# Kernel optimization log

Measured on AMD Instinct MI355X. Metric: run time of the kernel, lower is better.

## Reference

```python
import jax, jax.numpy as jnp
import numpy as np

N, D, E = 100000, 128, 1600000
BN_SCALE = 1.0 / np.sqrt(1.0 + 1e-3)  # Keras BN at inference with init stats: x/sqrt(var+eps)


def bn(x):
    return x * jnp.asarray(BN_SCALE, x.dtype)


def l2norm(x):
    s = jnp.sum(x * x, axis=1, keepdims=True)
    return x * jax.lax.rsqrt(jnp.maximum(s, 1e-12))


def spmm(rows, cols, vals, h, n):
    # (sparse NxN) @ (dense NxD) via gather + segment_sum
    return jax.ops.segment_sum(vals[:, None] * h[cols], rows, num_segments=n)


def setup_inputs() -> dict:
    key = jax.random.key(0)
    ks = jax.random.split(key, 12)
    g = 1.0 / np.sqrt(D)  # glorot-ish scale
    return {
        "x": jax.random.normal(ks[0], (N, D), jnp.float32),
        "a1_rows": jax.random.randint(ks[1], (E,), 0, N, jnp.int32),
        "a1_cols": jax.random.randint(ks[2], (E,), 0, N, jnp.int32),
        "a1_vals": jax.random.uniform(ks[3], (E,), jnp.float32),
        "a2_rows": jax.random.randint(ks[4], (E,), 0, N, jnp.int32),
        "a2_cols": jax.random.randint(ks[5], (E,), 0, N, jnp.int32),
        "a2_vals": jnp.ones((E,), jnp.float32),
        "w_gcn1": jax.random.normal(ks[6], (D, D), jnp.float32) * g,
        "b_gcn1": jnp.zeros((D,), jnp.float32),
        "w_att": jax.random.normal(ks[7], (D, D), jnp.float32) * g,
        "m1": jax.random.normal(ks[8], (D, D), jnp.float32) * g,
        "m2": jax.random.normal(ks[9], (D, D), jnp.float32) * g,
        "w_hw": jax.random.normal(ks[10], (D, D), jnp.float32) * g,
        "w_gcn2": jax.random.normal(ks[11], (D, D), jnp.float32) * g,
        "b_gcn2": jnp.zeros((D,), jnp.float32),
    }


def gcn_layer(x, rows, cols, vals, w, b, n):
    xb = bn(x)
    return jnp.tanh(spmm(rows, cols, vals, xb @ w, n) + b)


def atten_layer(x, rows, cols, vals, w, m1, m2, n):
    xb = bn(x)
    mapped = xb @ w  # [N, D]
    s1 = jnp.tanh(jnp.sum((xb @ m1) * xb, axis=1))  # [N]
    s2 = jnp.tanh(jnp.sum((xb @ m2) * xb, axis=1))  # [N]
    # per-edge score: A*s1[row] + A^T-broadcast s2[col], then leaky_relu (tf alpha=0.2)
    e = jax.nn.leaky_relu(vals * s1[rows] + vals * s2[cols], negative_slope=0.2)
    # sparse row-wise softmax
    mx = jax.ops.segment_max(e, rows, num_segments=n)
    ex = jnp.exp(e - mx[rows])
    denom = jax.ops.segment_sum(ex, rows, num_segments=n)
    a = ex / denom[rows]
    return spmm(rows, cols, a / jnp.maximum(vals, 1e-30) * vals * 0 + a, mapped, n) if False else jax.ops.segment_sum(a[:, None] * mapped[cols], rows, num_segments=n)


def highway_layer(y_att, y_gcn, w):
    i1 = bn(y_att)
    i2 = bn(y_gcn)
    gate = jax.nn.relu(jnp.tanh(i1 @ w))
    return jnp.tanh(i2 * (1.0 - gate) + i1 * gate)


def reference(x, a1_rows, a1_cols, a1_vals, a2_rows, a2_cols, a2_vals,
              w_gcn1, b_gcn1, w_att, m1, m2, w_hw, w_gcn2, b_gcn2):
    n = x.shape[0]
    y1 = gcn_layer(x, a1_rows, a1_cols, a1_vals, w_gcn1, b_gcn1, n)
    y2 = atten_layer(x, a2_rows, a2_cols, a2_vals, w_att, m1, m2, n)
    y3 = highway_layer(y2, y1, w_hw)
    y4 = gcn_layer(y3, a1_rows, a1_cols, a1_vals, w_gcn2, b_gcn2, n)
    y = jnp.concatenate([l2norm(y3), l2norm(y4), l2norm(x)], axis=1)
    return l2norm(y)
```

## Files before the change

kernel.cpp:

```cpp
#include <hip/hip_runtime.h>
#include <hip/hip_fp16.h>
#include <math.h>
#include <stdint.h>

#define DD 128
#define BSH 9

typedef _Float16 f16;
typedef _Float16 f16x8 __attribute__((ext_vector_type(8)));
typedef float f32x4 __attribute__((ext_vector_type(4)));

__global__ void k_hist(const int* __restrict__ r1, const int* __restrict__ r2,
                       int* __restrict__ hist, int E, int tile, int nt){
  __shared__ int h1[256], h2[256];
  int t = threadIdx.x;
  h1[t]=0; h2[t]=0; __syncthreads();
  int e0 = blockIdx.x*tile, e1 = min(e0+tile, E);
  for(int e=e0+t; e<e1; e+=256){
    atomicAdd(&h1[r1[e]>>BSH], 1);
    atomicAdd(&h2[r2[e]>>BSH], 1);
  }
  __syncthreads();
  hist[(size_t)blockIdx.x*256 + t] = h1[t];
  hist[(size_t)nt*256 + (size_t)blockIdx.x*256 + t] = h2[t];
}

__global__ void k_colscan(int* __restrict__ hist, int* __restrict__ colsum, int nt){
  __shared__ int sh[256];
  int g = blockIdx.x>>8, b = blockIdx.x&255;
  int t = threadIdx.x;
  int* H = hist + (size_t)g*nt*256;
  int v = (t<nt)? H[(size_t)t*256+b] : 0;
  sh[t]=v; __syncthreads();
  for(int off=1; off<256; off<<=1){
    int add = (t>=off)? sh[t-off] : 0;
    __syncthreads(); sh[t]+=add; __syncthreads();
  }
  if(t<nt) H[(size_t)t*256+b] = sh[t]-v;
  if(t==255) colsum[g*256+b] = sh[255];
}

__global__ void k_basescan(const int* __restrict__ colsum, int* __restrict__ base){
  __shared__ int sh[512];
  int t = threadIdx.x;
  int g = t>>8, st = t&255;
  int v = colsum[t];
  sh[t]=v; __syncthreads();
  for(int off=1; off<256; off<<=1){
    int add = (st>=off)? sh[t-off] : 0;
    __syncthreads(); sh[t]+=add; __syncthreads();
  }
  base[g*257+st] = sh[t]-v;
  if(st==255) base[g*257+256] = sh[t];
}

__global__ void k_partition(const int* __restrict__ r1, const int* __restrict__ c1, const float* __restrict__ v1,
                            const int* __restrict__ r2, const int* __restrict__ c2,
                            const int* __restrict__ hist, const int* __restrict__ base,
                            int2* __restrict__ st1, int* __restrict__ st2, int E, int tile, int nt){
  __shared__ int l1[256], l2[256];
  int t = threadIdx.x;
  l1[t]=0; l2[t]=0; __syncthreads();
  int bx = blockIdx.x;
  int e0 = bx*tile, e1e = min(e0+tile, E);
  const int* off1 = hist + (size_t)bx*256;
  const int* off2 = hist + (size_t)nt*256 + (size_t)bx*256;
  for(int e=e0+t; e<e1e; e+=256){
    {
      int r = r1[e]; int b = r>>BSH;
      int rank = atomicAdd(&l1[b], 1);
      int dst = base[b] + off1[b] + rank;
      st1[dst] = make_int2(((r - (b<<BSH))<<17) | c1[e], __float_as_int(v1[e]));
    }
    {
      int r = r2[e]; int b = r>>BSH;
      int rank = atomicAdd(&l2[b], 1);
      int dst = base[257+b] + off2[b] + rank;
      st2[dst] = ((r - (b<<BSH))<<17) | c2[e];
    }
  }
}

__global__ void k_csr_bucket(const int2* __restrict__ st1, const int* __restrict__ st2,
                             const int* __restrict__ base,
                             int2* __restrict__ e1, int* __restrict__ e2,
                             int* __restrict__ rs, int N, int nbk){
  __shared__ int cnt[512];
  __shared__ int cur[512];
  __shared__ int sc[256];
  int g = blockIdx.x / nbk;
  int b = blockIdx.x % nbk;
  int t = threadIdx.x;
  cnt[t]=0; cnt[256+t]=0;
  __syncthreads();
  int ebeg = base[g*257+b], eend = base[g*257+b+1];
  if(g==0){
    for(int i=ebeg+t; i<eend; i+=256) atomicAdd(&cnt[st1[i].x>>17], 1);
  } else {
    for(int i=ebeg+t; i<eend; i+=256) atomicAdd(&cnt[st2[i]>>17], 1);
  }
  __syncthreads();
  int a0 = cnt[2*t], a1 = cnt[2*t+1];
  int s = a0+a1;
  sc[t]=s; __syncthreads();
  for(int off=1; off<256; off<<=1){
    int add = (t>=off)? sc[t-off] : 0;
    __syncthreads(); sc[t]+=add; __syncthreads();
  }
  int ex = sc[t]-s;
  cur[2*t] = ex; cur[2*t+1] = ex + a0;
  __syncthreads();
  int r0 = b<<BSH;
  int* rsg = rs + (size_t)g*(N+1);
  for(int i=t; i<512; i+=256){
    int r = r0+i;
    if(r<N) rsg[r] = ebeg + cur[i];
  }
  if(b==nbk-1 && t==0) rsg[N] = base[g*257+256];
  __syncthreads();
  if(g==0){
    for(int i=ebeg+t; i<eend; i+=256){
      int2 w = st1[i];
      int lr = w.x>>17;
      int p = ebeg + atomicAdd(&cur[lr], 1);
      e1[p] = make_int2(w.x & 0x1FFFF, w.y);
    }
  } else {
    for(int i=ebeg+t; i<eend; i+=256){
      int w = st2[i];
      int lr = w>>17;
      int p = ebeg + atomicAdd(&cur[lr], 1);
      e2[p] = w & 0x1FFFF;
    }
  }
}

__global__ void k_wprep(const float* __restrict__ w0, const float* __restrict__ w1,
                        const float* __restrict__ w2, const float* __restrict__ w3,
                        const float* __restrict__ w4, const float* __restrict__ w5,
                        f16* __restrict__ wh){
  __shared__ __align__(16) f16 tw[128][136];
  int b = blockIdx.x, t = threadIdx.x;
  const float* W = (b==0)?w0:(b==1)?w1:(b==2)?w2:(b==3)?w3:(b==4)?w4:w5;
  for(int j=0;j<16;++j){
    int f = j*256+t; int k = f>>5, c4 = f&31;
    float4 v = *(const float4*)(W + (size_t)k*DD + c4*4);
    tw[c4*4+0][k]=(f16)v.x; tw[c4*4+1][k]=(f16)v.y; tw[c4*4+2][k]=(f16)v.z; tw[c4*4+3][k]=(f16)v.w;
  }
  __syncthreads();
  f16* dst = wh + (size_t)b*16384;
  for(int j=0;j<8;++j){
    int f = j*256+t; int c = f>>4, seg = f&15;
    *(int4*)&dst[(size_t)c*DD + seg*8] = *(int4*)&tw[c][seg*8];
  }
}

__global__ __launch_bounds__(256) void k_xgemms(
    const float* __restrict__ x, const f16* __restrict__ wh,
    f16* __restrict__ h1h, f16* __restrict__ mapped,
    float* __restrict__ s1, float* __restrict__ s2,
    float bn, float sscale, int n){
  __shared__ __align__(16) f16 at[64][136];
  __shared__ __align__(16) f16 wt[128][136];
  int t = threadIdx.x;
  int r0 = blockIdx.x*64;
  int l = t&63, w = t>>6, li = l&15, g = l>>4;
  for(int p=0;p<4;++p){
    int row = p*16 + (t>>4), seg = t&15;
    union{ f16 h[8]; int4 v; } u;
    u.v = make_int4(0,0,0,0);
    if(r0+row < n){
      const float* src = x + (size_t)(r0+row)*DD + seg*8;
      float4 a = *(const float4*)src, b = *(const float4*)(src+4);
      u.h[0]=(f16)a.x; u.h[1]=(f16)a.y; u.h[2]=(f16)a.z; u.h[3]=(f16)a.w;
      u.h[4]=(f16)b.x; u.h[5]=(f16)b.y; u.h[6]=(f16)b.z; u.h[7]=(f16)b.w;
    }
    *(int4*)&at[row][seg*8] = u.v;
  }
  for(int p=0;p<4;++p){
    __syncthreads();
    const f16* Wp = wh + (size_t)p*16384;
    for(int j=0;j<8;++j){
      int f = j*256+t; int c = f>>4, seg = f&15;
      *(int4*)&wt[c][seg*8] = *(const int4*)(Wp + (size_t)c*DD + seg*8);
    }
    __syncthreads();
    f32x4 acc[8];
    #pragma unroll
    for(int ct=0;ct<8;++ct) acc[ct] = (f32x4){0.f,0.f,0.f,0.f};
    #pragma unroll
    for(int ks=0;ks<4;++ks){
      f16x8 a = *(const f16x8*)&at[w*16+li][ks*32+g*8];
      #pragma unroll
      for(int ct=0;ct<8;++ct){
        f16x8 b = *(const f16x8*)&wt[ct*16+li][ks*32+g*8];
        acc[ct] = __builtin_amdgcn_mfma_f32_16x16x32_f16(a, b, acc[ct], 0,0,0);
      }
    }
    if(p<2){
      f16* out = p ? mapped : h1h;
      __syncthreads();
      #pragma unroll
      for(int ct=0;ct<8;++ct)
        #pragma unroll
        for(int reg=0;reg<4;++reg)
          wt[w*16+g*4+reg][ct*16+li] = (f16)(acc[ct][reg]*bn);
      __syncthreads();
      for(int j=0;j<4;++j){
        int f = j*256+t; int row = f>>4, seg = f&15;
        if(r0+row < n) *(int4*)&out[(size_t)(r0+row)*DD + seg*8] = *(int4*)&wt[row][seg*8];
      }
    } else {
      float* sd = (p==2) ? s1 : s2;
      #pragma unroll
      for(int reg=0;reg<4;++reg){
        float pd = 0.f;
        #pragma unroll
        for(int ct=0;ct<8;++ct)
          pd += acc[ct][reg]*(float)at[w*16+g*4+reg][ct*16+li];
        pd += __shfl_xor(pd,1,64); pd += __shfl_xor(pd,2,64);
        pd += __shfl_xor(pd,4,64); pd += __shfl_xor(pd,8,64);
        if(li==0){
          int grow = r0 + w*16 + g*4 + reg;
          if(grow < n) sd[grow] = tanhf(sscale*pd);
        }
      }
    }
  }
}

__global__ __launch_bounds__(256) void k_hw2(
    const f16* __restrict__ y2h, const f16* __restrict__ y1h,
    const f16* __restrict__ wh, f16* __restrict__ y3h, f16* __restrict__ h3h,
    float bn, int n){
  __shared__ __align__(16) f16 at[64][136];
  __shared__ __align__(16) f16 wt[128][136];
  int t = threadIdx.x;
  int r0 = blockIdx.x*64;
  int l = t&63, w = t>>6, li = l&15, g = l>>4;
  for(int p=0;p<4;++p){
    int row = p*16 + (t>>4), seg = t&15;
    int4 v = make_int4(0,0,0,0);
    if(r0+row < n) v = *(const int4*)(y2h + (size_t)(r0+row)*DD + seg*8);
    *(int4*)&at[row][seg*8] = v;
  }
  __syncthreads();
  for(int j=0;j<8;++j){
    int f = j*256+t; int c = f>>4, seg = f&15;
    *(int4*)&wt[c][seg*8] = *(const int4*)(wh + (size_t)4*16384 + (size_t)c*DD + seg*8);
  }
  __syncthreads();
  f32x4 acc[8];
  #pragma unroll
  for(int ct=0;ct<8;++ct) acc[ct] = (f32x4){0.f,0.f,0.f,0.f};
  #pragma unroll
  for(int ks=0;ks<4;++ks){
    f16x8 a = *(const f16x8*)&at[w*16+li][ks*32+g*8];
    #pragma unroll
    for(int ct=0;ct<8;++ct){
      f16x8 b = *(const f16x8*)&wt[ct*16+li][ks*32+g*8];
      acc[ct] = __builtin_amdgcn_mfma_f32_16x16x32_f16(a, b, acc[ct], 0,0,0);
    }
  }
  float res[8][4];
  #pragma unroll
  for(int ct=0;ct<8;++ct)
    #pragma unroll
    for(int reg=0;reg<4;++reg){
      int lrow = w*16+g*4+reg, col = ct*16+li;
      int grow = r0+lrow;
      float gt = tanhf(bn*acc[ct][reg]); gt = fmaxf(gt, 0.f);
      float y1v = (grow<n)? (float)y1h[(size_t)grow*DD+col] : 0.f;
      float y2v = (float)at[lrow][col];
      res[ct][reg] = tanhf(bn*(y1v*(1.f-gt) + y2v*gt));
    }
  #pragma unroll
  for(int ct=0;ct<8;++ct)
    #pragma unroll
    for(int reg=0;reg<4;++reg)
      at[w*16+g*4+reg][ct*16+li] = (f16)res[ct][reg];
  __syncthreads();
  for(int j=0;j<4;++j){
    int f = j*256+t; int row = f>>4, seg = f&15;
    if(r0+row < n) *(int4*)&y3h[(size_t)(r0+row)*DD + seg*8] = *(int4*)&at[row][seg*8];
  }
  __syncthreads();
  for(int j=0;j<8;++j){
    int f = j*256+t; int c = f>>4, seg = f&15;
    *(int4*)&wt[c][seg*8] = *(const int4*)(wh + (size_t)5*16384 + (size_t)c*DD + seg*8);
  }
  __syncthreads();
  #pragma unroll
  for(int ct=0;ct<8;++ct) acc[ct] = (f32x4){0.f,0.f,0.f,0.f};
  #pragma unroll
  for(int ks=0;ks<4;++ks){
    f16x8 a = *(const f16x8*)&at[w*16+li][ks*32+g*8];
    #pragma unroll
    for(int ct=0;ct<8;++ct){
      f16x8 b = *(const f16x8*)&wt[ct*16+li][ks*32+g*8];
      acc[ct] = __builtin_amdgcn_mfma_f32_16x16x32_f16(a, b, acc[ct], 0,0,0);
    }
  }
  __syncthreads();
  #pragma unroll
  for(int ct=0;ct<8;++ct)
    #pragma unroll
    for(int reg=0;reg<4;++reg)
      wt[w*16+g*4+reg][ct*16+li] = (f16)(acc[ct][reg]*bn);
  __syncthreads();
  for(int j=0;j<4;++j){
    int f = j*256+t; int row = f>>4, seg = f&15;
    if(r0+row < n) *(int4*)&h3h[(size_t)(r0+row)*DD + seg*8] = *(int4*)&wt[row][seg*8];
  }
}

__device__ __forceinline__ void spmm_row(const int* __restrict__ rs, const int2* __restrict__ e1,
                                         const __half* __restrict__ h, const float* __restrict__ bias,
                                         __half* __restrict__ out, int row, int lane){
  int beg = rs[row], end = rs[row+1];
  float ax=0.f, ay=0.f;
  int k = beg;
  for(; k+8<=end; k+=8){
    int2 cv[8]; __half2 hh[8];
    #pragma unroll
    for(int j=0;j<8;++j) cv[j] = e1[k+j];
    #pragma unroll
    for(int j=0;j<8;++j) hh[j] = ((const __half2*)(h + (size_t)cv[j].x*DD))[lane];
    #pragma unroll
    for(int j=0;j<8;++j){
      float v = __int_as_float(cv[j].y);
      float2 f = __half22float2(hh[j]);
      ax += v*f.x; ay += v*f.y;
    }
  }
  for(; k<end; ++k){
    int2 cv = e1[k];
    float v = __int_as_float(cv.y);
    float2 f = __half22float2(((const __half2*)(h + (size_t)cv.x*DD))[lane]);
    ax += v*f.x; ay += v*f.y;
  }
  float2 b = ((const float2*)bias)[lane];
  ((__half2*)(out + (size_t)row*DD))[lane] = __floats2half2_rn(tanhf(ax+b.x), tanhf(ay+b.y));
}

__device__ __forceinline__ void attn_row(const int* __restrict__ rs, const int* __restrict__ e2,
                                         const float* __restrict__ s1, const float* __restrict__ s2,
                                         const __half* __restrict__ mapped, __half* __restrict__ out,
                                         int row, int lane){
  int beg = rs[row], end = rs[row+1];
  float s1r = s1[row];
  float ax=0.f, ay=0.f, den=0.f;
  int k = beg;
  for(; k+8<=end; k+=8){
    int cs[8]; float sv[8]; __half2 mh[8];
    #pragma unroll
    for(int j=0;j<8;++j) cs[j] = e2[k+j];
    #pragma unroll
    for(int j=0;j<8;++j) sv[j] = s2[cs[j]];
    #pragma unroll
    for(int j=0;j<8;++j) mh[j] = ((const __half2*)(mapped + (size_t)cs[j]*DD))[lane];
    #pragma unroll
    for(int j=0;j<8;++j){
      float e = s1r + sv[j]; e = (e>=0.f)? e : 0.2f*e;
      float ex = __expf(e);
      float2 f = __half22float2(mh[j]);
      den += ex; ax += ex*f.x; ay += ex*f.y;
    }
  }
  for(; k<end; ++k){
    int c = e2[k];
    float e = s1r + s2[c]; e = (e>=0.f)? e : 0.2f*e;
    float ex = __expf(e);
    float2 f = __half22float2(((const __half2*)(mapped + (size_t)c*DD))[lane]);
    den += ex; ax += ex*f.x; ay += ex*f.y;
  }
  float inv = (end > beg) ? 1.0f/den : 0.0f;
  ((__half2*)(out + (size_t)row*DD))[lane] = __floats2half2_rn(ax*inv, ay*inv);
}

__global__ void k_agg1(const int* __restrict__ rs, const int2* __restrict__ e1,
                       const __half* __restrict__ h1h, const float* __restrict__ b1, __half* __restrict__ y1h,
                       const int* __restrict__ e2, const float* __restrict__ s1, const float* __restrict__ s2,
                       const __half* __restrict__ mapped, __half* __restrict__ y2h,
                       int n, int gR){
  int lane = threadIdx.x & 63;
  if((int)blockIdx.x < gR){
    int row = blockIdx.x*4 + (threadIdx.x>>6);
    if(row>=n) return;
    spmm_row(rs, e1, h1h, b1, y1h, row, lane);
  } else {
    int row = (blockIdx.x-gR)*4 + (threadIdx.x>>6);
    if(row>=n) return;
    attn_row(rs+(n+1), e2, s1, s2, mapped, y2h, row, lane);
  }
}

__global__ void k_spmm2(const int* __restrict__ rs, const int2* __restrict__ e1,
                        const __half* __restrict__ h, const float* __restrict__ bias,
                        __half* __restrict__ out, int n){
  int row = blockIdx.x*4 + (threadIdx.x>>6);
  if(row>=n) return;
  spmm_row(rs, e1, h, bias, out, row, threadIdx.x & 63);
}

__global__ void k_final(const __half* __restrict__ y3, const __half* __restrict__ y4,
                        const float* __restrict__ x, float* __restrict__ out, int n){
  int row = blockIdx.x*4 + (threadIdx.x>>6);
  if(row>=n) return;
  int lane = threadIdx.x & 63;
  float2 a = __half22float2(((const __half2*)(y3 + (size_t)row*DD))[lane]);
  float2 b = __half22float2(((const __half2*)(y4 + (size_t)row*DD))[lane]);
  float2 c = ((const float2*)(x  + (size_t)row*DD))[lane];
  float sa = a.x*a.x + a.y*a.y;
  float sb = b.x*b.x + b.y*b.y;
  float sc = c.x*c.x + c.y*c.y;
  #pragma unroll
  for(int off=32; off; off>>=1){
    sa += __shfl_xor(sa, off, 64);
    sb += __shfl_xor(sb, off, 64);
    sc += __shfl_xor(sc, off, 64);
  }
  float ia = rsqrtf(fmaxf(sa, 1e-12f));
  float ib = rsqrtf(fmaxf(sb, 1e-12f));
  float ic = rsqrtf(fmaxf(sc, 1e-12f));
  float tot = sa*ia*ia + sb*ib*ib + sc*ic*ic;
  float f = rsqrtf(fmaxf(tot, 1e-12f));
  float fa = ia*f, fb = ib*f, fc = ic*f;
  float2* o = (float2*)(out + (size_t)row*(3*DD));
  o[lane]     = make_float2(a.x*fa, a.y*fa);
  o[64+lane]  = make_float2(b.x*fb, b.y*fb);
  o[128+lane] = make_float2(c.x*fc, c.y*fc);
}

extern "C" void kernel_launch(void* const* d_in, const int* in_sizes, int n_in,
                              void* d_out, int out_size, void* d_ws, size_t ws_size,
                              hipStream_t stream){
  const float* x   = (const float*)d_in[0];
  const int*   a1r = (const int*)d_in[1];
  const int*   a1c = (const int*)d_in[2];
  const float* a1v = (const float*)d_in[3];
  const int*   a2r = (const int*)d_in[4];
  const int*   a2c = (const int*)d_in[5];
  const float* w1  = (const float*)d_in[7];
  const float* b1  = (const float*)d_in[8];
  const float* watt= (const float*)d_in[9];
  const float* m1  = (const float*)d_in[10];
  const float* m2  = (const float*)d_in[11];
  const float* whw = (const float*)d_in[12];
  const float* w2  = (const float*)d_in[13];
  const float* b2  = (const float*)d_in[14];

  const int N = in_sizes[0]/DD;
  const int E = in_sizes[1];
  const float BN = (float)(1.0/sqrt(1.0+1e-3));
  const size_t NB = (size_t)N*DD;

  int tile = 8192, nt = (E+tile-1)/tile;
  while(nt > 256){ tile <<= 1; nt = (E+tile-1)/tile; }
  const int nbk = (N + (1<<BSH) - 1) >> BSH;

  f16* Bh = (f16*)d_ws;
  f16* Ch = Bh + NB;
  f16* Dh = Ch + NB;
  f16* Eh = Dh + NB;
  f16* wh = Eh + NB;
  float* s1 = (float*)(wh + 6*16384);
  float* s2 = s1 + N;
  int*  rs  = (int*)(s2 + N);
  uintptr_t pa = ((uintptr_t)(rs + 2*(N+1)) + 15) & ~(uintptr_t)15;
  int2* e1  = (int2*)pa;
  int*  e2  = (int*)(e1 + E);
  int*  hist = e2 + E;
  int*  colsum = hist + (size_t)2*nt*256;
  int*  base = colsum + 512;

  int2* st1 = (int2*)Bh;
  int*  st2 = (int*)(st1 + E);

  const int gR = (N+3)/4;
  const int gM = (N+63)/64;
  float* out = (float*)d_out;

  k_wprep<<<6,256,0,stream>>>(w1, watt, m1, m2, whw, w2, wh);

  k_hist<<<nt,256,0,stream>>>(a1r, a2r, hist, E, tile, nt);
  k_colscan<<<512,256,0,stream>>>(hist, colsum, nt);
  k_basescan<<<1,512,0,stream>>>(colsum, base);
  k_partition<<<nt,256,0,stream>>>(a1r,a1c,a1v, a2r,a2c, hist, base, st1, st2, E, tile, nt);
  k_csr_bucket<<<2*nbk,256,0,stream>>>(st1, st2, base, e1, e2, rs, N, nbk);

  k_xgemms<<<gM,256,0,stream>>>(x, wh, Bh, Ch, s1, s2, BN, BN*BN, N);

  k_agg1<<<2*gR,256,0,stream>>>(rs, e1, (const __half*)Bh, b1, (__half*)Dh,
                                e2, s1, s2, (const __half*)Ch, (__half*)Eh, N, gR);

  k_hw2<<<gM,256,0,stream>>>(Eh, Dh, wh, Ch, Bh, BN, N);

  k_spmm2<<<gR,256,0,stream>>>(rs, e1, (const __half*)Bh, b2, (__half*)Dh, N);

  k_final<<<gR,256,0,stream>>>((const __half*)Ch, (const __half*)Dh, x, out, N);
}
```

Before: 497.3 us.

## Co-schedule weight prep with histogram and GEMMs with partition; half-wave row aggregation

Merges the weight-conversion kernel into the histogram launch and the dense x-GEMM kernel into the edge-partition launch, using block-index ranges so independent work shares one grid. The partition staging buffers move out of the Bh region into their own workspace so the GEMM can write Bh at the same time. SpMM and attention aggregation now use 32 lanes per row with 8-byte loads and 8 rows per block, and handle the tail with clamped, masked loads instead of a scalar remainder loop. This cuts launch count and idle tail time and raises per-lane memory width. In exchange it uses more workspace memory and does some wasted loads on partial batches.

```diff
diff --git a/kernel.cpp b/kernel.cpp
--- a/kernel.cpp
+++ b/kernel.cpp
@@ -10,19 +10,42 @@
 typedef _Float16 f16x8 __attribute__((ext_vector_type(8)));
 typedef float f32x4 __attribute__((ext_vector_type(4)));
 
-__global__ void k_hist(const int* __restrict__ r1, const int* __restrict__ r2,
-                       int* __restrict__ hist, int E, int tile, int nt){
-  __shared__ int h1[256], h2[256];
+__global__ __launch_bounds__(256) void k_ph(
+    const float* __restrict__ w0, const float* __restrict__ w1, const float* __restrict__ w2,
+    const float* __restrict__ w3, const float* __restrict__ w4, const float* __restrict__ w5,
+    f16* __restrict__ wh,
+    const int* __restrict__ r1, const int* __restrict__ r2, int* __restrict__ hist,
+    int E, int tile, int nt){
+  __shared__ __align__(16) unsigned char smem[128*136*2];
   int t = threadIdx.x;
-  h1[t]=0; h2[t]=0; __syncthreads();
-  int e0 = blockIdx.x*tile, e1 = min(e0+tile, E);
-  for(int e=e0+t; e<e1; e+=256){
-    atomicAdd(&h1[r1[e]>>BSH], 1);
-    atomicAdd(&h2[r2[e]>>BSH], 1);
-  }
-  __syncthreads();
-  hist[(size_t)blockIdx.x*256 + t] = h1[t];
-  hist[(size_t)nt*256 + (size_t)blockIdx.x*256 + t] = h2[t];
+  if((int)blockIdx.x < 6){
+    auto tw = (f16 (*)[136])smem;
+    int b = blockIdx.x;
+    const float* W = (b==0)?w0:(b==1)?w1:(b==2)?w2:(b==3)?w3:(b==4)?w4:w5;
+    for(int j=0;j<16;++j){
+      int f = j*256+t; int k = f>>5, c4 = f&31;
+      float4 v = *(const float4*)(W + (size_t)k*DD + c4*4);
+      tw[c4*4+0][k]=(f16)v.x; tw[c4*4+1][k]=(f16)v.y; tw[c4*4+2][k]=(f16)v.z; tw[c4*4+3][k]=(f16)v.w;
+    }
+    __syncthreads();
+    f16* dst = wh + (size_t)b*16384;
+    for(int j=0;j<8;++j){
+      int f = j*256+t; int c = f>>4, seg = f&15;
+      *(int4*)&dst[(size_t)c*DD + seg*8] = *(int4*)&tw[c][seg*8];
+    }
+  } else {
+    int* h1 = (int*)smem; int* h2 = h1+256;
+    h1[t]=0; h2[t]=0; __syncthreads();
+    int hb = blockIdx.x - 6;
+    int e0 = hb*tile, e1 = min(e0+tile, E);
+    for(int e=e0+t; e<e1; e+=256){
+      atomicAdd(&h1[r1[e]>>BSH], 1);
+      atomicAdd(&h2[r2[e]>>BSH], 1);
+    }
+    __syncthreads();
+    hist[(size_t)hb*256 + t] = h1[t];
+    hist[(size_t)nt*256 + (size_t)hb*256 + t] = h2[t];
+  }
 }
 
 __global__ void k_colscan(int* __restrict__ hist, int* __restrict__ colsum, int nt){
@@ -54,29 +77,104 @@
   if(st==255) base[g*257+256] = sh[t];
 }
 
-__global__ void k_partition(const int* __restrict__ r1, const int* __restrict__ c1, const float* __restrict__ v1,
-                            const int* __restrict__ r2, const int* __restrict__ c2,
-                            const int* __restrict__ hist, const int* __restrict__ base,
-                            int2* __restrict__ st1, int* __restrict__ st2, int E, int tile, int nt){
-  __shared__ int l1[256], l2[256];
+__global__ __launch_bounds__(256) void k_px(
+    const int* __restrict__ r1, const int* __restrict__ c1, const float* __restrict__ v1,
+    const int* __restrict__ r2, const int* __restrict__ c2,
+    const int* __restrict__ hist, const int* __restrict__ base,
+    int2* __restrict__ st1, int* __restrict__ st2, int E, int tile, int nt,
+    const float* __restrict__ x, const f16* __restrict__ wh,
+    f16* __restrict__ h1h, f16* __restrict__ mapped,
+    float* __restrict__ s1, float* __restrict__ s2,
+    float bn, float sscale, int n){
+  __shared__ __align__(16) unsigned char smem[52224];
   int t = threadIdx.x;
-  l1[t]=0; l2[t]=0; __syncthreads();
-  int bx = blockIdx.x;
-  int e0 = bx*tile, e1e = min(e0+tile, E);
-  const int* off1 = hist + (size_t)bx*256;
-  const int* off2 = hist + (size_t)nt*256 + (size_t)bx*256;
-  for(int e=e0+t; e<e1e; e+=256){
-    {
-      int r = r1[e]; int b = r>>BSH;
-      int rank = atomicAdd(&l1[b], 1);
-      int dst = base[b] + off1[b] + rank;
-      st1[dst] = make_int2(((r - (b<<BSH))<<17) | c1[e], __float_as_int(v1[e]));
-    }
-    {
-      int r = r2[e]; int b = r>>BSH;
-      int rank = atomicAdd(&l2[b], 1);
-      int dst = base[257+b] + off2[b] + rank;
-      st2[dst] = ((r - (b<<BSH))<<17) | c2[e];
+  if((int)blockIdx.x < nt){
+    int* l1 = (int*)smem; int* l2 = l1+256;
+    l1[t]=0; l2[t]=0; __syncthreads();
+    int bx = blockIdx.x;
+    int e0 = bx*tile, e1e = min(e0+tile, E);
+    const int* off1 = hist + (size_t)bx*256;
+    const int* off2 = hist + (size_t)nt*256 + (size_t)bx*256;
+    for(int e=e0+t; e<e1e; e+=256){
+      {
+        int r = r1[e]; int b = r>>BSH;
+        int rank = atomicAdd(&l1[b], 1);
+        int dst = base[b] + off1[b] + rank;
+        st1[dst] = make_int2(((r - (b<<BSH))<<17) | c1[e], __float_as_int(v1[e]));
+      }
+      {
+        int r = r2[e]; int b = r>>BSH;
+        int rank = atomicAdd(&l2[b], 1);
+        int dst = base[257+b] + off2[b] + rank;
+        st2[dst] = ((r - (b<<BSH))<<17) | c2[e];
+      }
+    }
+  } else {
+    auto at = (f16 (*)[136])smem;
+    auto wt = (f16 (*)[136])(smem + 64*136*2);
+    int r0 = (blockIdx.x - nt)*64;
+    int l = t&63, w = t>>6, li = l&15, g = l>>4;
+    for(int p=0;p<4;++p){
+      int row = p*16 + (t>>4), seg = t&15;
+      union{ f16 h[8]; int4 v; } u;
+      u.v = make_int4(0,0,0,0);
+      if(r0+row < n){
+        const float* src = x + (size_t)(r0+row)*DD + seg*8;
+        float4 a = *(const float4*)src, b = *(const float4*)(src+4);
+        u.h[0]=(f16)a.x; u.h[1]=(f16)a.y; u.h[2]=(f16)a.z; u.h[3]=(f16)a.w;
+        u.h[4]=(f16)b.x; u.h[5]=(f16)b.y; u.h[6]=(f16)b.z; u.h[7]=(f16)b.w;
+      }
+      *(int4*)&at[row][seg*8] = u.v;
+    }
+    for(int p=0;p<4;++p){
+      __syncthreads();
+      const f16* Wp = wh + (size_t)p*16384;
+      for(int j=0;j<8;++j){
+        int f = j*256+t; int c = f>>4, seg = f&15;
+        *(int4*)&wt[c][seg*8] = *(const int4*)(Wp + (size_t)c*DD + seg*8);
+      }
+      __syncthreads();
+      f32x4 acc[8];
+      #pragma unroll
+      for(int ct=0;ct<8;++ct) acc[ct] = (f32x4){0.f,0.f,0.f,0.f};
+      #pragma unroll
+      for(int ks=0;ks<4;++ks){
+        f16x8 a = *(const f16x8*)&at[w*16+li][ks*32+g*8];
+        #pragma unroll
+        for(int ct=0;ct<8;++ct){
+          f16x8 b = *(const f16x8*)&wt[ct*16+li][ks*32+g*8];
+          acc[ct] = __builtin_amdgcn_mfma_f32_16x16x32_f16(a, b, acc[ct], 0,0,0);
+        }
+      }
+      if(p<2){
+        f16* out = p ? mapped : h1h;
+        __syncthreads();
+        #pragma unroll
+        for(int ct=0;ct<8;++ct)
+          #pragma unroll
+          for(int reg=0;reg<4;++reg)
+            wt[w*16+g*4+reg][ct*16+li] = (f16)(acc[ct][reg]*bn);
+        __syncthreads();
+        for(int j=0;j<4;++j){
+          int f = j*256+t; int row = f>>4, seg = f&15;
+          if(r0+row < n) *(int4*)&out[(size_t)(r0+row)*DD + seg*8] = *(int4*)&wt[row][seg*8];
+        }
+      } else {
+        float* sd = (p==2) ? s1 : s2;
+        #pragma unroll
+        for(int reg=0;reg<4;++reg){
+          float pd = 0.f;
+          #pragma unroll
+          for(int ct=0;ct<8;++ct)
+            pd += acc[ct][reg]*(float)at[w*16+g*4+reg][ct*16+li];
+          pd += __shfl_xor(pd,1,64); pd += __shfl_xor(pd,2,64);
+          pd += __shfl_xor(pd,4,64); pd += __shfl_xor(pd,8,64);
+          if(li==0){
+            int grow = r0 + w*16 + g*4 + reg;
+            if(grow < n) sd[grow] = tanhf(sscale*pd);
+          }
+        }
+      }
     }
   }
 }
@@ -131,100 +229,6 @@
       int lr = w>>17;
       int p = ebeg + atomicAdd(&cur[lr], 1);
       e2[p] = w & 0x1FFFF;
-    }
-  }
-}
-
-__global__ void k_wprep(const float* __restrict__ w0, const float* __restrict__ w1,
-                        const float* __restrict__ w2, const float* __restrict__ w3,
-                        const float* __restrict__ w4, const float* __restrict__ w5,
-                        f16* __restrict__ wh){
-  __shared__ __align__(16) f16 tw[128][136];
-  int b = blockIdx.x, t = threadIdx.x;
-  const float* W = (b==0)?w0:(b==1)?w1:(b==2)?w2:(b==3)?w3:(b==4)?w4:w5;
-  for(int j=0;j<16;++j){
-    int f = j*256+t; int k = f>>5, c4 = f&31;
-    float4 v = *(const float4*)(W + (size_t)k*DD + c4*4);
-    tw[c4*4+0][k]=(f16)v.x; tw[c4*4+1][k]=(f16)v.y; tw[c4*4+2][k]=(f16)v.z; tw[c4*4+3][k]=(f16)v.w;
-  }
-  __syncthreads();
-  f16* dst = wh + (size_t)b*16384;
-  for(int j=0;j<8;++j){
-    int f = j*256+t; int c = f>>4, seg = f&15;
-    *(int4*)&dst[(size_t)c*DD + seg*8] = *(int4*)&tw[c][seg*8];
-  }
-}
-
-__global__ __launch_bounds__(256) void k_xgemms(
-    const float* __restrict__ x, const f16* __restrict__ wh,
-    f16* __restrict__ h1h, f16* __restrict__ mapped,
-    float* __restrict__ s1, float* __restrict__ s2,
-    float bn, float sscale, int n){
-  __shared__ __align__(16) f16 at[64][136];
-  __shared__ __align__(16) f16 wt[128][136];
-  int t = threadIdx.x;
-  int r0 = blockIdx.x*64;
-  int l = t&63, w = t>>6, li = l&15, g = l>>4;
-  for(int p=0;p<4;++p){
-    int row = p*16 + (t>>4), seg = t&15;
-    union{ f16 h[8]; int4 v; } u;
-    u.v = make_int4(0,0,0,0);
-    if(r0+row < n){
-      const float* src = x + (size_t)(r0+row)*DD + seg*8;
-      float4 a = *(const float4*)src, b = *(const float4*)(src+4);
-      u.h[0]=(f16)a.x; u.h[1]=(f16)a.y; u.h[2]=(f16)a.z; u.h[3]=(f16)a.w;
-      u.h[4]=(f16)b.x; u.h[5]=(f16)b.y; u.h[6]=(f16)b.z; u.h[7]=(f16)b.w;
-    }
-    *(int4*)&at[row][seg*8] = u.v;
-  }
-  for(int p=0;p<4;++p){
-    __syncthreads();
-    const f16* Wp = wh + (size_t)p*16384;
-    for(int j=0;j<8;++j){
-      int f = j*256+t; int c = f>>4, seg = f&15;
-      *(int4*)&wt[c][seg*8] = *(const int4*)(Wp + (size_t)c*DD + seg*8);
-    }
-    __syncthreads();
-    f32x4 acc[8];
-    #pragma unroll
-    for(int ct=0;ct<8;++ct) acc[ct] = (f32x4){0.f,0.f,0.f,0.f};
-    #pragma unroll
-    for(int ks=0;ks<4;++ks){
-      f16x8 a = *(const f16x8*)&at[w*16+li][ks*32+g*8];
-      #pragma unroll
-      for(int ct=0;ct<8;++ct){
-        f16x8 b = *(const f16x8*)&wt[ct*16+li][ks*32+g*8];
-        acc[ct] = __builtin_amdgcn_mfma_f32_16x16x32_f16(a, b, acc[ct], 0,0,0);
-      }
-    }
-    if(p<2){
-      f16* out = p ? mapped : h1h;
-      __syncthreads();
-      #pragma unroll
-      for(int ct=0;ct<8;++ct)
-        #pragma unroll
-        for(int reg=0;reg<4;++reg)
-          wt[w*16+g*4+reg][ct*16+li] = (f16)(acc[ct][reg]*bn);
-      __syncthreads();
-      for(int j=0;j<4;++j){
-        int f = j*256+t; int row = f>>4, seg = f&15;
-        if(r0+row < n) *(int4*)&out[(size_t)(r0+row)*DD + seg*8] = *(int4*)&wt[row][seg*8];
-      }
-    } else {
-      float* sd = (p==2) ? s1 : s2;
-      #pragma unroll
-      for(int reg=0;reg<4;++reg){
-        float pd = 0.f;
-        #pragma unroll
-        for(int ct=0;ct<8;++ct)
-          pd += acc[ct][reg]*(float)at[w*16+g*4+reg][ct*16+li];
-        pd += __shfl_xor(pd,1,64); pd += __shfl_xor(pd,2,64);
-        pd += __shfl_xor(pd,4,64); pd += __shfl_xor(pd,8,64);
-        if(li==0){
-          int grow = r0 + w*16 + g*4 + reg;
-          if(grow < n) sd[grow] = tanhf(sscale*pd);
-        }
-      }
     }
   }
 }
@@ -314,93 +318,91 @@
   }
 }
 
-__device__ __forceinline__ void spmm_row(const int* __restrict__ rs, const int2* __restrict__ e1,
-                                         const __half* __restrict__ h, const float* __restrict__ bias,
-                                         __half* __restrict__ out, int row, int lane){
+__device__ __forceinline__ void spmm_row32(const int* __restrict__ rs, const int2* __restrict__ e1,
+                                           const __half* __restrict__ h, const float* __restrict__ bias,
+                                           __half* __restrict__ out, int row, int l ){
   int beg = rs[row], end = rs[row+1];
-  float ax=0.f, ay=0.f;
-  int k = beg;
-  for(; k+8<=end; k+=8){
-    int2 cv[8]; __half2 hh[8];
-    #pragma unroll
-    for(int j=0;j<8;++j) cv[j] = e1[k+j];
-    #pragma unroll
-    for(int j=0;j<8;++j) hh[j] = ((const __half2*)(h + (size_t)cv[j].x*DD))[lane];
-    #pragma unroll
-    for(int j=0;j<8;++j){
-      float v = __int_as_float(cv[j].y);
-      float2 f = __half22float2(hh[j]);
-      ax += v*f.x; ay += v*f.y;
-    }
-  }
-  for(; k<end; ++k){
-    int2 cv = e1[k];
-    float v = __int_as_float(cv.y);
-    float2 f = __half22float2(((const __half2*)(h + (size_t)cv.x*DD))[lane]);
-    ax += v*f.x; ay += v*f.y;
-  }
-  float2 b = ((const float2*)bias)[lane];
-  ((__half2*)(out + (size_t)row*DD))[lane] = __floats2half2_rn(tanhf(ax+b.x), tanhf(ay+b.y));
-}
-
-__device__ __forceinline__ void attn_row(const int* __restrict__ rs, const int* __restrict__ e2,
-                                         const float* __restrict__ s1, const float* __restrict__ s2,
-                                         const __half* __restrict__ mapped, __half* __restrict__ out,
-                                         int row, int lane){
+  float a0=0.f, a1=0.f, a2=0.f, a3=0.f;
+  if(end > beg){
+    for(int k=beg; k<end; k+=8){
+      int2 cv[8]; uint2 hh[8];
+      #pragma unroll
+      for(int j=0;j<8;++j){ int kk = min(k+j, end-1); cv[j] = e1[kk]; }
+      #pragma unroll
+      for(int j=0;j<8;++j) hh[j] = ((const uint2*)(h + (size_t)cv[j].x*DD))[l];
+      #pragma unroll
+      for(int j=0;j<8;++j){
+        float v = (k+j<end)? __int_as_float(cv[j].y) : 0.f;
+        float2 f0 = __half22float2(*(__half2*)&hh[j].x);
+        float2 f1 = __half22float2(*(__half2*)&hh[j].y);
+        a0 += v*f0.x; a1 += v*f0.y; a2 += v*f1.x; a3 += v*f1.y;
+      }
+    }
+  }
+  float4 b4 = ((const float4*)bias)[l];
+  __half2 o0 = __floats2half2_rn(tanhf(a0+b4.x), tanhf(a1+b4.y));
+  __half2 o1 = __floats2half2_rn(tanhf(a2+b4.z), tanhf(a3+b4.w));
+  uint2 u; u.x = *(unsigned*)&o0; u.y = *(unsigned*)&o1;
+  ((uint2*)(out + (size_t)row*DD))[l] = u;
+}
+
+__device__ __forceinline__ void attn_row32(const int* __restrict__ rs, const int* __restrict__ e2,
+                                           const float* __restrict__ s1, const float* __restrict__ s2,
+                                           const __half* __restrict__ mapped, __half* __restrict__ out,
+                                           int row, int l){
   int beg = rs[row], end = rs[row+1];
   float s1r = s1[row];
-  float ax=0.f, ay=0.f, den=0.f;
-  int k = beg;
-  for(; k+8<=end; k+=8){
-    int cs[8]; float sv[8]; __half2 mh[8];
-    #pragma unroll
-    for(int j=0;j<8;++j) cs[j] = e2[k+j];
-    #pragma unroll
-    for(int j=0;j<8;++j) sv[j] = s2[cs[j]];
-    #pragma unroll
-    for(int j=0;j<8;++j) mh[j] = ((const __half2*)(mapped + (size_t)cs[j]*DD))[lane];
-    #pragma unroll
-    for(int j=0;j<8;++j){
-      float e = s1r + sv[j]; e = (e>=0.f)? e : 0.2f*e;
-      float ex = __expf(e);
-      float2 f = __half22float2(mh[j]);
-      den += ex; ax += ex*f.x; ay += ex*f.y;
-    }
-  }
-  for(; k<end; ++k){
-    int c = e2[k];
-    float e = s1r + s2[c]; e = (e>=0.f)? e : 0.2f*e;
-    float ex = __expf(e);
-    float2 f = __half22float2(((const __half2*)(mapped + (size_t)c*DD))[lane]);
-    den += ex; ax += ex*f.x; ay += ex*f.y;
+  float a0=0.f, a1=0.f, a2=0.f, a3=0.f, den=0.f;
+  if(end > beg){
+    for(int k=beg; k<end; k+=8){
+      int cs[8]; float sv[8]; uint2 mh[8];
+      #pragma unroll
+      for(int j=0;j<8;++j){ int kk = min(k+j, end-1); cs[j] = e2[kk]; }
+      #pragma unroll
+      for(int j=0;j<8;++j) sv[j] = s2[cs[j]];
+      #pragma unroll
+      for(int j=0;j<8;++j) mh[j] = ((const uint2*)(mapped + (size_t)cs[j]*DD))[l];
+      #pragma unroll
+      for(int j=0;j<8;++j){
+        float e = s1r + sv[j]; e = (e>=0.f)? e : 0.2f*e;
+        float ex = (k+j<end)? __expf(e) : 0.f;
+        float2 f0 = __half22float2(*(__half2*)&mh[j].x);
+        float2 f1 = __half22float2(*(__half2*)&mh[j].y);
+        den += ex;
+        a0 += ex*f0.x; a1 += ex*f0.y; a2 += ex*f1.x; a3 += ex*f1.y;
+      }
+    }
   }
   float inv = (end > beg) ? 1.0f/den : 0.0f;
-  ((__half2*)(out + (size_t)row*DD))[lane] = __floats2half2_rn(ax*inv, ay*inv);
+  __half2 o0 = __floats2half2_rn(a0*inv, a1*inv);
+  __half2 o1 = __floats2half2_rn(a2*inv, a3*inv);
+  uint2 u; u.x = *(unsigned*)&o0; u.y = *(unsigned*)&o1;
+  ((uint2*)(out + (size_t)row*DD))[l] = u;
 }
 
 __global__ void k_agg1(const int* __restrict__ rs, const int2* __restrict__ e1,
                        const __half* __restrict__ h1h, const float* __restrict__ b1, __half* __restrict__ y1h,
                        const int* __restrict__ e2, const float* __restrict__ s1, const float* __restrict__ s2,
                        const __half* __restrict__ mapped, __half* __restrict__ y2h,
-                       int n, int gR){
-  int lane = threadIdx.x & 63;
-  if((int)blockIdx.x < gR){
-    int row = blockIdx.x*4 + (threadIdx.x>>6);
+                       int n, int gS){
+  int l = threadIdx.x & 31;
+  if((int)blockIdx.x < gS){
+    int row = blockIdx.x*8 + (threadIdx.x>>5);
     if(row>=n) return;
-    spmm_row(rs, e1, h1h, b1, y1h, row, lane);
+    spmm_row32(rs, e1, h1h, b1, y1h, row, l);
   } else {
-    int row = (blockIdx.x-gR)*4 + (threadIdx.x>>6);
+    int row = (blockIdx.x-gS)*8 + (threadIdx.x>>5);
     if(row>=n) return;
-    attn_row(rs+(n+1), e2, s1, s2, mapped, y2h, row, lane);
+    attn_row32(rs+(n+1), e2, s1, s2, mapped, y2h, row, l);
   }
 }
 
 __global__ void k_spmm2(const int* __restrict__ rs, const int2* __restrict__ e1,
                         const __half* __restrict__ h, const float* __restrict__ bias,
                         __half* __restrict__ out, int n){
-  int row = blockIdx.x*4 + (threadIdx.x>>6);
+  int row = blockIdx.x*8 + (threadIdx.x>>5);
   if(row>=n) return;
-  spmm_row(rs, e1, h, bias, out, row, threadIdx.x & 63);
+  spmm_row32(rs, e1, h, bias, out, row, threadIdx.x & 31);
 }
 
 __global__ void k_final(const __half* __restrict__ y3, const __half* __restrict__ y4,
@@ -470,33 +472,34 @@
   uintptr_t pa = ((uintptr_t)(rs + 2*(N+1)) + 15) & ~(uintptr_t)15;
   int2* e1  = (int2*)pa;
   int*  e2  = (int*)(e1 + E);
-  int*  hist = e2 + E;
+  uintptr_t pb = ((uintptr_t)(e2 + E) + 15) & ~(uintptr_t)15;
+  int2* st1 = (int2*)pb;
+  int*  st2 = (int*)(st1 + E);
+  int*  hist = st2 + E;
   int*  colsum = hist + (size_t)2*nt*256;
   int*  base = colsum + 512;
 
-  int2* st1 = (int2*)Bh;
-  int*  st2 = (int*)(st1 + E);
-
   const int gR = (N+3)/4;
+  const int gS = (N+7)/8;
   const int gM = (N+63)/64;
   float* out = (float*)d_out;
 
-  k_wprep<<<6,256,0,stream>>>(w1, watt, m1, m2, whw, w2, wh);
-
-  k_hist<<<nt,256,0,stream>>>(a1r, a2r, hist, E, tile, nt);
+  k_ph<<<6+nt,256,0,stream>>>(w1, watt, m1, m2, whw, w2, wh, a1r, a2r, hist, E, tile, nt);
+
   k_colscan<<<512,256,0,stream>>>(hist, colsum, nt);
   k_basescan<<<1,512,0,stream>>>(colsum, base);
-  k_partition<<<nt,256,0,stream>>>(a1r,a1c,a1v, a2r,a2c, hist, base, st1, st2, E, tile, nt);
+
+  k_px<<<nt+gM,256,0,stream>>>(a1r,a1c,a1v, a2r,a2c, hist, base, st1, st2, E, tile, nt,
+                               x, wh, Bh, Ch, s1, s2, BN, BN*BN, N);
+
   k_csr_bucket<<<2*nbk,256,0,stream>>>(st1, st2, base, e1, e2, rs, N, nbk);
 
-  k_xgemms<<<gM,256,0,stream>>>(x, wh, Bh, Ch, s1, s2, BN, BN*BN, N);
-
-  k_agg1<<<2*gR,256,0,stream>>>(rs, e1, (const __half*)Bh, b1, (__half*)Dh,
-                                e2, s1, s2, (const __half*)Ch, (__half*)Eh, N, gR);
+  k_agg1<<<2*gS,256,0,stream>>>(rs, e1, (const __half*)Bh, b1, (__half*)Dh,
+                                e2, s1, s2, (const __half*)Ch, (__half*)Eh, N, gS);
 
   k_hw2<<<gM,256,0,stream>>>(Eh, Dh, wh, Ch, Bh, BN, N);
 
-  k_spmm2<<<gR,256,0,stream>>>(rs, e1, (const __half*)Bh, b2, (__half*)Dh, N);
+  k_spmm2<<<gS,256,0,stream>>>(rs, e1, (const __half*)Bh, b2, (__half*)Dh, N);
 
   k_final<<<gR,256,0,stream>>>((const __half*)Ch, (const __half*)Dh, x, out, N);
 }
```

Result: faster. 438.3 us (-11.9%).
